# Kernel optimization log

Measured on AMD Instinct MI355X. Metric: run time of the kernel, lower is better.

Reference implementation:

```python
import math
import jax, jax.numpy as jnp
import numpy as np

# hyperparameters (module defaults; w_scale overridden to 1.0)
EMA_SPEED = 0.05
REW_SENS = 1.0
LR = 0.0033
MOMENTUM = 0.4
UNTANH = 0.6
SPEED = 0.5
WIDTH = 0.1
WD = 0.01
LAT_DECAY = 0.01
NOISE_SCALE = 0.8
C_MOMENT = 0.99
W_SCALE = 1.0


def rms_norm(x, axis=-1):
    return x * jax.lax.rsqrt(jnp.mean(x * x, axis=axis, keepdims=True) + 1e-6)


def setup_inputs() -> dict:
    key = jax.random.key(0)
    ks = jax.random.split(key, 16)
    B, N, D = 16, 128, 64
    s = 1.0 / math.sqrt(D)
    return {
        'eye_env': jax.random.normal(ks[0], (B, D), jnp.float32),
        'stomach_env': jax.random.normal(ks[1], (B, D), jnp.float32),
        'state': jax.random.normal(ks[2], (B, N, D), jnp.float32),
        'output': jax.random.normal(ks[3], (B, N, D), jnp.float32),
        'W1': jax.random.normal(ks[4], (B, N, D, D), jnp.float32) * s,
        'W2': jax.random.normal(ks[5], (B, N, D, D), jnp.float32) * s,
        'W3': jax.random.normal(ks[6], (B, N, D, D), jnp.float32) * s,
        'M1': jax.random.normal(ks[7], (B, N, D, D), jnp.float32) * 0.2,
        'M2': jax.random.normal(ks[8], (B, N, D, D), jnp.float32) * 0.2,
        'M3': jax.random.normal(ks[9], (B, N, D, D), jnp.float32) * 0.2,
        'E_baseline': jax.random.uniform(ks[10], (B, N, D), jnp.float32),
        'A': jax.nn.softmax(jax.random.normal(ks[11], (B, N, N), jnp.float32), axis=2),
        'noise_A': jax.random.normal(ks[12], (B, N, N), jnp.float32),
        'noise1_raw': jax.random.normal(ks[13], (B, N, D), jnp.float32),
        'noise2_raw': jax.random.normal(ks[14], (B, N, D), jnp.float32),
        'step_counter': 0,
    }


def reference(eye_env, stomach_env, state, output, W1, W2, W3, M1, M2, M3,
              E_baseline, A, noise_A, noise1_raw, noise2_raw, step_counter):
    B, N, D = state.shape
    sc = jnp.float32(step_counter) + 1.0  # self.step_counter += 1

    # attention routing
    q = jnp.einsum('bnj,bnjk->bnk', state, W3)
    k = jnp.einsum('bnj,bnjk->bnk', state, W2)
    raw_A = jnp.einsum('bnd,bmd->bnm', q, k) / math.sqrt(D) + noise_A * 1e-5
    P_dense = jax.nn.softmax(raw_A, axis=2)
    keep = (P_dense > 1.0 / (N + 1.0)) | (P_dense == jnp.max(P_dense, axis=2, keepdims=True))
    P = jax.nn.softmax(jnp.where(keep, raw_A, -jnp.inf), axis=2)
    A_new = A * C_MOMENT + P * (1.0 - C_MOMENT)
    A_new = A_new.at[:, 0:2, :].set(0.0)

    # message passing + sensory clamp
    target = jnp.einsum('bnm,bmd->bnd', A_new, output)
    target = target.at[:, 0].set(eye_env).at[:, 1].set(stomach_env)

    # prediction
    raw_pred = jnp.einsum('bnj,bnjk->bnk', state, W1)
    raw = raw_pred - jnp.tanh(raw_pred) * UNTANH
    prediction = jnp.tanh(raw) * math.sqrt(2.0 + math.sqrt(2.0))

    err = prediction - target
    E_curr = jax.nn.softmax(err, axis=-1)
    bmask = (E_baseline == 0).astype(jnp.float32)
    Eb = E_baseline * (1.0 - bmask) + E_curr * bmask
    Eb = Eb * (1.0 - EMA_SPEED) + EMA_SPEED * E_curr
    advantage = E_curr - Eb
    R = -rms_norm(advantage[..., None] * REW_SENS)  # (B,N,D,1)
    mask = (Eb > 0).astype(jnp.float32)[..., None]

    # noise injection
    state_mag = jnp.sum(jnp.abs(state), axis=(-2, -1), keepdims=True)
    noise1 = noise1_raw / (1.0 + state_mag)
    noise2 = noise2_raw * jnp.std(err, ddof=1) * NOISE_SCALE
    noisy_state = state + noise1 + noise2

    # Hebbian outer-product gradient, G_NORM=1.0 -> rms-normalized
    lg = -jnp.einsum('bni,bnj->bnij', err, noisy_state)
    lg = rms_norm(lg, axis=(2, 3))

    plasticity = 1.0 - R
    grad1 = plasticity * lg * mask + LAT_DECAY * W3 - WD * W1
    grad2 = plasticity * lg * mask + LAT_DECAY * W1 - WD * W2
    grad3 = plasticity * lg * mask + LAT_DECAY * W2 - WD * W3

    # travelling gaussian column mask
    idx = jnp.arange(D, dtype=jnp.float32).reshape(1, 1, 1, D)
    center = (sc * SPEED) % D
    diff = jnp.abs(idx - center)
    diff = jnp.minimum(diff, D - diff)
    g_mask = jnp.exp(-diff ** 2 / (2.0 * WIDTH ** 2 + 1e-6))

    M1n = M1 * MOMENTUM + (1.0 - MOMENTUM) * (grad1 * g_mask)
    M2n = M2 * MOMENTUM + (1.0 - MOMENTUM) * (grad2 * g_mask)
    M3n = M3 * MOMENTUM + (1.0 - MOMENTUM) * (grad3 * g_mask)
    W1n = rms_norm(W1 + LR * M1n) * W_SCALE
    W2n = rms_norm(W2 + LR * M2n) * W_SCALE
    W3n = rms_norm(W3 + LR * M3n) * W_SCALE

    # new output = prediction, new state = target
    return prediction, target, A_new, W1n, W2n, W3n
```

## Files before the change

kernel.cpp:

```cpp
#include <hip/hip_runtime.h>
#include <hip/hip_bf16.h>

typedef __hip_bfloat16 bf16;
typedef float f32x4 __attribute__((ext_vector_type(4)));

__device__ __forceinline__ float b2f(bf16 x) { return __bfloat162float(x); }

template<bool F32>
__device__ __forceinline__ float ld(const void* p, size_t i) {
  if constexpr (F32) return ((const float*)p)[i];
  else return b2f(((const bf16*)p)[i]);
}

template<bool F32>
__device__ __forceinline__ void ld4(const void* p, size_t i, float v[4]) {
  if constexpr (F32) {
    const float4 a = *(const float4*)((const float*)p + i);
    v[0]=a.x; v[1]=a.y; v[2]=a.z; v[3]=a.w;
  } else {
    union { uint2 u; bf16 h[4]; } t;
    t.u = *(const uint2*)((const bf16*)p + i);
    #pragma unroll
    for (int c = 0; c < 4; ++c) v[c] = b2f(t.h[c]);
  }
}

template<bool F32>
__device__ __forceinline__ void ld8(const void* p, size_t i, float v[8]) {
  if constexpr (F32) {
    const float4 a = *(const float4*)((const float*)p + i);
    const float4 b = *(const float4*)((const float*)p + i + 4);
    v[0]=a.x; v[1]=a.y; v[2]=a.z; v[3]=a.w;
    v[4]=b.x; v[5]=b.y; v[6]=b.z; v[7]=b.w;
  } else {
    union { uint4 u; bf16 h[8]; } t;
    t.u = *(const uint4*)((const bf16*)p + i);
    #pragma unroll
    for (int c = 0; c < 8; ++c) v[c] = b2f(t.h[c]);
  }
}

template<bool F32>
__device__ __forceinline__ void ld8nt(const void* p, size_t i, float v[8]) {
  if constexpr (F32) {
    const f32x4* q = (const f32x4*)((const float*)p + i);
    const f32x4 a = __builtin_nontemporal_load(q);
    const f32x4 b = __builtin_nontemporal_load(q + 1);
    v[0]=a[0]; v[1]=a[1]; v[2]=a[2]; v[3]=a[3];
    v[4]=b[0]; v[5]=b[1]; v[6]=b[2]; v[7]=b[3];
  } else {
    ld8<false>(p, i, v);
  }
}

__device__ __forceinline__ float plast(float Ec, float Ebl) {
  const float Eb0 = (Ebl == 0.f) ? Ec : Ebl;
  const float Eb  = Eb0 * 0.95f + 0.05f * Ec;
  const float adv = Ec - Eb;
  const float R   = -adv * rsqrtf(adv*adv + 1e-6f);
  return (Eb > 0.f) ? (1.f - R) : 0.f;
}


template<bool F32>
__device__ __forceinline__ void k1_wave(
    const void* state, const void* W1, const void* W2, const void* W3,
    float* qw, float* kw, float* mag, float* out_pred, int node, int lane)
{
  const int b = node >> 7;
  const float st = ld<F32>(state, (size_t)node*64 + lane);
  float am = fabsf(st);
  #pragma unroll
  for (int s = 32; s; s >>= 1) am += __shfl_xor(am, s, 64);
  if (lane == 0) atomicAdd(&mag[b], am);

  const int jg = lane >> 4, cq = lane & 15;
  const int c0 = cq * 4;
  const size_t nb = (size_t)node * 4096;
  float aq[4] = {0,0,0,0}, ak[4] = {0,0,0,0}, ap[4] = {0,0,0,0};
  #pragma unroll 4
  for (int jj = 0; jj < 16; ++jj) {
    const int j = jg*16 + jj;
    const float sj = __shfl(st, j, 64);
    const size_t o = nb + (size_t)j*64 + c0;
    float wv[4];
    ld4<F32>(W3, o, wv);
    #pragma unroll
    for (int cc = 0; cc < 4; ++cc) aq[cc] += sj * wv[cc];
    ld4<F32>(W2, o, wv);
    #pragma unroll
    for (int cc = 0; cc < 4; ++cc) ak[cc] += sj * wv[cc];
    ld4<F32>(W1, o, wv);
    #pragma unroll
    for (int cc = 0; cc < 4; ++cc) ap[cc] += sj * wv[cc];
  }
  #pragma unroll
  for (int cc = 0; cc < 4; ++cc) {
    aq[cc] += __shfl_xor(aq[cc], 16, 64); aq[cc] += __shfl_xor(aq[cc], 32, 64);
    ak[cc] += __shfl_xor(ak[cc], 16, 64); ak[cc] += __shfl_xor(ak[cc], 32, 64);
    ap[cc] += __shfl_xor(ap[cc], 16, 64); ap[cc] += __shfl_xor(ap[cc], 32, 64);
  }
  if (jg == 0) {
    *(float4*)(qw + (size_t)node*64 + c0) = make_float4(aq[0], aq[1], aq[2], aq[3]);
  } else if (jg == 1) {
    *(float4*)(kw + (size_t)node*64 + c0) = make_float4(ak[0], ak[1], ak[2], ak[3]);
  } else if (jg == 2) {
    float pr[4];
    #pragma unroll
    for (int cc = 0; cc < 4; ++cc) {
      const float raw = ap[cc] - tanhf(ap[cc]) * 0.6f;
      pr[cc] = tanhf(raw) * 1.8477590650225735f;
    }
    *(float4*)(out_pred + (size_t)node*64 + c0) = make_float4(pr[0], pr[1], pr[2], pr[3]);
  }
}

__global__ __launch_bounds__(256) void k1_qkpred(
    const void* __restrict__ state,
    const void* __restrict__ W1, const void* __restrict__ W2,
    const void* __restrict__ W3,
    float* __restrict__ qw, float* __restrict__ kw,
    float* __restrict__ mag, float* __restrict__ out_pred,
    int* __restrict__ flagws)
{
  const int tid = threadIdx.x;
  const int w = tid >> 6, lane = tid & 63;
  bool huge = false;
  for (int i = lane; i < 1024; i += 64) {
    const float x = b2f(((const bf16*)state)[i]);
    if (!(fabsf(x) < 1e5f)) huge = true;
  }
  const bool f32 = (__ballot(huge) != 0ull);
  if (blockIdx.x == 0 && tid == 0) *flagws = f32 ? 1 : 0;
  const int node = blockIdx.x * 4 + w;
  if (f32) k1_wave<true >(state, W1, W2, W3, qw, kw, mag, out_pred, node, lane);
  else     k1_wave<false>(state, W1, W2, W3, qw, kw, mag, out_pred, node, lane);
}

template<bool F32>
__device__ __forceinline__ void k2_body(
    const float* qw, const float* kw, const float* predw,
    const void* noiseA, const void* Aold, const void* outp,
    const void* eye, const void* stomach, const void* Ebase,
    float* errw, float* plw, float* stats,
    float* out_target, float* out_A,
    float* s_k, float* s_q, float* s_A)
{
  const int bidx = blockIdx.x;
  const int b = bidx >> 4;
  const int n0 = (bidx & 15) * 8;
  const int tid = threadIdx.x;

  {
    const float* kwb = kw + (size_t)b * 8192;
    #pragma unroll
    for (int it = 0; it < 8; ++it) {
      const int idx = it*256 + tid;
      const int m = idx >> 4, dq = idx & 15;
      const float4 v = *(const float4*)(kwb + (size_t)idx * 4);
      float* dst = &s_k[m*65 + dq*4];
      dst[0] = v.x; dst[1] = v.y; dst[2] = v.z; dst[3] = v.w;
    }
    if (tid < 128) {
      const int rr = tid >> 4, dq = tid & 15;
      *(float4*)&s_q[rr*64 + dq*4] =
          *(const float4*)(qw + ((size_t)(b*128 + n0 + rr))*64 + dq*4);
    }
  }
  __syncthreads();

  const int rr = tid >> 5, c = tid & 31;
  const int n = n0 + rr;
  const size_t node = (size_t)b*128 + n;

  float acc[4] = {0.f, 0.f, 0.f, 0.f};
  {
    const float* qrow = s_q + rr*64;
    #pragma unroll 8
    for (int j = 0; j < 64; ++j) {
      const float qv = qrow[j];
      acc[0] += qv * s_k[(c     )*65 + j];
      acc[1] += qv * s_k[(c + 32)*65 + j];
      acc[2] += qv * s_k[(c + 64)*65 + j];
      acc[3] += qv * s_k[(c + 96)*65 + j];
    }
  }
  float raw[4];
  #pragma unroll
  for (int i = 0; i < 4; ++i)
    raw[i] = acc[i]*0.125f + 1e-5f*ld<F32>(noiseA, node*128 + c + 32*i);

  float rmx = fmaxf(fmaxf(raw[0], raw[1]), fmaxf(raw[2], raw[3]));
  #pragma unroll
  for (int s = 16; s >= 1; s >>= 1) rmx = fmaxf(rmx, __shfl_xor(rmx, s, 64));
  float e[4], S = 0.f;
  #pragma unroll
  for (int i = 0; i < 4; ++i) { e[i] = expf(raw[i] - rmx); S += e[i]; }
  #pragma unroll
  for (int s = 16; s >= 1; s >>= 1) S += __shfl_xor(S, s, 64);
  float ek[4], Sk = 0.f;
  #pragma unroll
  for (int i = 0; i < 4; ++i) {
    const float Pd = e[i] / S;
    ek[i] = ((Pd > 0.007751937984496124f) || (raw[i] == rmx)) ? e[i] : 0.f;
    Sk += ek[i];
  }
  #pragma unroll
  for (int s = 16; s >= 1; s >>= 1) Sk += __shfl_xor(Sk, s, 64);
  #pragma unroll
  for (int i = 0; i < 4; ++i) {
    const int m = c + 32*i;
    const float P = ek[i] / Sk;
    const float An = (n < 2) ? 0.f
                   : 0.99f * ld<F32>(Aold, node*128 + m) + 0.01f * P;
    out_A[node*128 + m] = An;
    s_A[rr*128 + m] = An;
  }
  __syncthreads();

  float t0, t1;
  if (n == 0) {
    t0 = ld<F32>(eye, (size_t)b*64 + c);
    t1 = ld<F32>(eye, (size_t)b*64 + c + 32);
  } else if (n == 1) {
    t0 = ld<F32>(stomach, (size_t)b*64 + c);
    t1 = ld<F32>(stomach, (size_t)b*64 + c + 32);
  } else {
    t0 = 0.f; t1 = 0.f;
    const float* arow = s_A + rr*128;
    const size_t ob = (size_t)b * 8192;
    #pragma unroll 4
    for (int m = 0; m < 128; ++m) {
      const float a = arow[m];
      t0 += a * ld<F32>(outp, ob + m*64 + c);
      t1 += a * ld<F32>(outp, ob + m*64 + c + 32);
    }
  }
  out_target[node*64 + c]      = t0;
  out_target[node*64 + c + 32] = t1;
  const float e0 = predw[node*64 + c]      - t0;
  const float e1 = predw[node*64 + c + 32] - t1;
  errw[node*64 + c]      = e0;
  errw[node*64 + c + 32] = e1;

  float mx = fmaxf(e0, e1);
  #pragma unroll
  for (int s = 16; s >= 1; s >>= 1) mx = fmaxf(mx, __shfl_xor(mx, s, 64));
  const float x0 = expf(e0 - mx), x1 = expf(e1 - mx);
  float ss = x0 + x1;
  #pragma unroll
  for (int s = 16; s >= 1; s >>= 1) ss += __shfl_xor(ss, s, 64);
  plw[node*64 + c]      = plast(x0/ss, ld<F32>(Ebase, node*64 + c));
  plw[node*64 + c + 32] = plast(x1/ss, ld<F32>(Ebase, node*64 + c + 32));

  float se = e0 + e1, sq = e0*e0 + e1*e1;
  #pragma unroll
  for (int s = 16; s >= 1; s >>= 1) { se += __shfl_xor(se, s, 64); sq += __shfl_xor(sq, s, 64); }
  if (c == 0) { atomicAdd(&stats[0], se); atomicAdd(&stats[1], sq); }
}

__global__ __launch_bounds__(256) void k2_attn(
    const int* __restrict__ flag,
    const float* __restrict__ qw, const float* __restrict__ kw,
    const float* __restrict__ predw,
    const void* __restrict__ noiseA, const void* __restrict__ Aold,
    const void* __restrict__ outp,
    const void* __restrict__ eye, const void* __restrict__ stomach,
    const void* __restrict__ Ebase,
    float* __restrict__ errw, float* __restrict__ plw,
    float* __restrict__ stats,
    float* __restrict__ out_target, float* __restrict__ out_A)
{
  __shared__ alignas(16) float s_k[128*65];
  __shared__ alignas(16) float s_q[8*64];
  __shared__ alignas(16) float s_A[8*128];
  if (*flag) k2_body<true >(qw,kw,predw,noiseA,Aold,outp,eye,stomach,Ebase,errw,plw,stats,out_target,out_A,s_k,s_q,s_A);
  else       k2_body<false>(qw,kw,predw,noiseA,Aold,outp,eye,stomach,Ebase,errw,plw,stats,out_target,out_A,s_k,s_q,s_A);
}

template<bool F32>
__device__ __forceinline__ void k3_body(
    const float* errw, const float* plw,
    const void* state, const void* n1raw, const void* n2raw,
    const float* mag, const float* stats, const int* stepc,
    const void* W1, const void* W2, const void* W3,
    const void* M1, const void* M2, const void* M3,
    float* oW1, float* oW2, float* oW3)
{
  const int node = blockIdx.x;
  const int b = node >> 7;
  const int tid = threadIdx.x;
  const int lane = tid & 63;
  const int r = tid >> 3;
  const int l8 = tid & 7;

  const size_t sb = (size_t)node*64 + lane;
  const float e_i  = errw[sb];
  const float pl_i = plw[sb];
  const float st_i = ld<F32>(state, sb);
  const float n1_i = ld<F32>(n1raw, sb);
  const float n2_i = ld<F32>(n2raw, sb);
  const float magb = mag[b];
  const float S1 = stats[0], S2 = stats[1];
  const float scv = (float)stepc[0] + 1.f;

  const size_t off = (size_t)node*4096 + (size_t)r*64 + (size_t)l8*8;
  float w1v[8], w2v[8], w3v[8], m1v[8], m2v[8], m3v[8];
  ld8  <F32>(W1, off, w1v); ld8  <F32>(W2, off, w2v); ld8  <F32>(W3, off, w3v);
  ld8nt<F32>(M1, off, m1v); ld8nt<F32>(M2, off, m2v); ld8nt<F32>(M3, off, m3v);

  const float Mn = 131072.f;
  const float var = (S2 - S1*S1/Mn) / (Mn - 1.f);
  const float stdv = sqrtf(fmaxf(var, 0.f));
  const float ns_i = st_i + n1_i / (1.f + magb)
                   + n2_i * stdv * 0.8f;
  float e2 = e_i*e_i, q2 = ns_i*ns_i;
  #pragma unroll
  for (int s = 32; s; s >>= 1) { e2 += __shfl_xor(e2, s, 64); q2 += __shfl_xor(q2, s, 64); }
  const float c_i  = -ns_i * rsqrtf(e2 * q2 * (1.f/4096.f) + 1e-6f);
  const float pe_i = pl_i * e_i;
  const float center = fmodf(scv * 0.5f, 64.f);
  float dff = fabsf((float)lane - center);
  dff = fminf(dff, 64.f - dff);
  const float g_i = expf(-dff*dff * (1.f/0.020001f));

  const float pe = __shfl(pe_i, r, 64);
  float cj[8], gj[8];
  #pragma unroll
  for (int cc = 0; cc < 8; ++cc) {
    const int j = l8*8 + cc;
    cj[cc] = __shfl(c_i, j, 64);
    gj[cc] = __shfl(g_i, j, 64);
  }

  float t1[8], t2[8], t3[8];
  float ss1 = 0.f, ss2 = 0.f, ss3 = 0.f;
  #pragma unroll
  for (int cc = 0; cc < 8; ++cc) {
    const float lgterm = pe * cj[cc];
    const float g = gj[cc];
    const float g1 = lgterm + 0.01f*w3v[cc] - 0.01f*w1v[cc];
    const float g2 = lgterm + 0.01f*w1v[cc] - 0.01f*w2v[cc];
    const float g3 = lgterm + 0.01f*w2v[cc] - 0.01f*w3v[cc];
    const float v1 = w1v[cc] + 0.0033f*(0.4f*m1v[cc] + 0.6f*g1*g);
    const float v2 = w2v[cc] + 0.0033f*(0.4f*m2v[cc] + 0.6f*g2*g);
    const float v3 = w3v[cc] + 0.0033f*(0.4f*m3v[cc] + 0.6f*g3*g);
    t1[cc] = v1; t2[cc] = v2; t3[cc] = v3;
    ss1 += v1*v1; ss2 += v2*v2; ss3 += v3*v3;
  }
  #pragma unroll
  for (int s = 1; s <= 4; s <<= 1) {
    ss1 += __shfl_xor(ss1, s, 64);
    ss2 += __shfl_xor(ss2, s, 64);
    ss3 += __shfl_xor(ss3, s, 64);
  }
  const float r1 = rsqrtf(ss1*(1.f/64.f) + 1e-6f);
  const float r2 = rsqrtf(ss2*(1.f/64.f) + 1e-6f);
  const float r3 = rsqrtf(ss3*(1.f/64.f) + 1e-6f);
  *(float4*)(oW1 + off)     = make_float4(t1[0]*r1, t1[1]*r1, t1[2]*r1, t1[3]*r1);
  *(float4*)(oW1 + off + 4) = make_float4(t1[4]*r1, t1[5]*r1, t1[6]*r1, t1[7]*r1);
  *(float4*)(oW2 + off)     = make_float4(t2[0]*r2, t2[1]*r2, t2[2]*r2, t2[3]*r2);
  *(float4*)(oW2 + off + 4) = make_float4(t2[4]*r2, t2[5]*r2, t2[6]*r2, t2[7]*r2);
  *(float4*)(oW3 + off)     = make_float4(t3[0]*r3, t3[1]*r3, t3[2]*r3, t3[3]*r3);
  *(float4*)(oW3 + off + 4) = make_float4(t3[4]*r3, t3[5]*r3, t3[6]*r3, t3[7]*r3);
}

__global__ __launch_bounds__(512) void k3_update(
    const int* __restrict__ flag,
    const float* __restrict__ errw, const float* __restrict__ plw,
    const void* __restrict__ state, const void* __restrict__ n1raw,
    const void* __restrict__ n2raw,
    const float* __restrict__ mag, const float* __restrict__ stats,
    const int* __restrict__ stepc,
    const void* __restrict__ W1, const void* __restrict__ W2,
    const void* __restrict__ W3,
    const void* __restrict__ M1, const void* __restrict__ M2,
    const void* __restrict__ M3,
    float* __restrict__ oW1, float* __restrict__ oW2, float* __restrict__ oW3)
{
  if (*flag) k3_body<true >(errw,plw,state,n1raw,n2raw,mag,stats,stepc,W1,W2,W3,M1,M2,M3,oW1,oW2,oW3);
  else       k3_body<false>(errw,plw,state,n1raw,n2raw,mag,stats,stepc,W1,W2,W3,M1,M2,M3,oW1,oW2,oW3);
}

extern "C" void kernel_launch(void* const* d_in, const int* in_sizes, int n_in,
                              void* d_out, int out_size, void* d_ws, size_t ws_size,
                              hipStream_t stream) {
  const void* eye     = d_in[0];
  const void* stomach = d_in[1];
  const void* state   = d_in[2];
  const void* outp    = d_in[3];
  const void* W1      = d_in[4];
  const void* W2      = d_in[5];
  const void* W3      = d_in[6];
  const void* M1      = d_in[7];
  const void* M2      = d_in[8];
  const void* M3      = d_in[9];
  const void* Ebase   = d_in[10];
  const void* Aold    = d_in[11];
  const void* noiseA  = d_in[12];
  const void* n1raw   = d_in[13];
  const void* n2raw   = d_in[14];
  const int*  stepc   = (const int*)d_in[15];

  float* ws    = (float*)d_ws;
  float* qw    = ws;
  float* kw    = ws + 131072;
  float* errw  = ws + 262144;
  float* plw   = ws + 393216;
  float* mag   = ws + 524288;
  float* stats = ws + 524304;
  int*   flag  = (int*)(ws + 524306);

  float* out        = (float*)d_out;
  float* out_pred   = out;
  float* out_target = out + 131072;
  float* out_A      = out + 262144;
  float* oW1        = out + 524288;
  float* oW2        = out + 8912896;
  float* oW3        = out + 17301504;

  hipMemsetAsync(mag, 0, 18 * sizeof(float), stream);
  k1_qkpred<<<512, 256, 0, stream>>>(state, W1, W2, W3, qw, kw, mag, out_pred, flag);
  k2_attn<<<256, 256, 0, stream>>>(flag, qw, kw, out_pred, noiseA, Aold, outp,
                                   eye, stomach, Ebase, errw, plw, stats,
                                   out_target, out_A);
  k3_update<<<2048, 512, 0, stream>>>(flag, errw, plw, state, n1raw, n2raw, mag, stats,
                                      stepc, W1, W2, W3, M1, M2, M3, oW1, oW2, oW3);
}
```

Baseline: 358.6 us.

## Split qk/pred projection into one wave per matrix and drop memset

The first kernel now assigns one wave per (node, matrix) pair, launching three times as many blocks. Each lane issues eight vector loads before consuming them, to raise memory-level parallelism on the W reads. The per-batch |state| sum no longer uses atomics: each node writes its own partial, and the attention kernel reduces the partials. The stats accumulators are zeroed inside the first kernel, which removes the separate memset launch. In exchange, every wave reloads and reshuffles state, and more waves are launched.

After: 333.3 us. 1.08x faster.

```diff
diff --git a/kernel.cpp b/kernel.cpp
--- a/kernel.cpp
+++ b/kernel.cpp
@@ -65,53 +65,56 @@
 template<bool F32>
 __device__ __forceinline__ void k1_wave(
     const void* state, const void* W1, const void* W2, const void* W3,
-    float* qw, float* kw, float* mag, float* out_pred, int node, int lane)
-{
-  const int b = node >> 7;
+    float* qw, float* kw, float* magn, float* out_pred,
+    int node, int mat, int lane)
+{
   const float st = ld<F32>(state, (size_t)node*64 + lane);
-  float am = fabsf(st);
-  #pragma unroll
-  for (int s = 32; s; s >>= 1) am += __shfl_xor(am, s, 64);
-  if (lane == 0) atomicAdd(&mag[b], am);
-
   const int jg = lane >> 4, cq = lane & 15;
   const int c0 = cq * 4;
-  const size_t nb = (size_t)node * 4096;
-  float aq[4] = {0,0,0,0}, ak[4] = {0,0,0,0}, ap[4] = {0,0,0,0};
-  #pragma unroll 4
-  for (int jj = 0; jj < 16; ++jj) {
-    const int j = jg*16 + jj;
-    const float sj = __shfl(st, j, 64);
-    const size_t o = nb + (size_t)j*64 + c0;
-    float wv[4];
-    ld4<F32>(W3, o, wv);
-    #pragma unroll
-    for (int cc = 0; cc < 4; ++cc) aq[cc] += sj * wv[cc];
-    ld4<F32>(W2, o, wv);
-    #pragma unroll
-    for (int cc = 0; cc < 4; ++cc) ak[cc] += sj * wv[cc];
-    ld4<F32>(W1, o, wv);
-    #pragma unroll
-    for (int cc = 0; cc < 4; ++cc) ap[cc] += sj * wv[cc];
+  const size_t nb = (size_t)node*4096 + (size_t)jg*1024 + c0;
+  const void* W = (mat == 0) ? W3 : (mat == 1) ? W2 : W1;
+
+  float acc[4] = {0.f, 0.f, 0.f, 0.f};
+  float buf[8][4];
+  #pragma unroll
+  for (int jj = 0; jj < 8; ++jj) ld4<F32>(W, nb + (size_t)jj*64, buf[jj]);
+  #pragma unroll
+  for (int jj = 0; jj < 8; ++jj) {
+    const float sj = __shfl(st, jg*16 + jj, 64);
+    #pragma unroll
+    for (int cc = 0; cc < 4; ++cc) acc[cc] += sj * buf[jj][cc];
+  }
+  #pragma unroll
+  for (int jj = 0; jj < 8; ++jj) ld4<F32>(W, nb + (size_t)(jj + 8)*64, buf[jj]);
+  #pragma unroll
+  for (int jj = 0; jj < 8; ++jj) {
+    const float sj = __shfl(st, jg*16 + 8 + jj, 64);
+    #pragma unroll
+    for (int cc = 0; cc < 4; ++cc) acc[cc] += sj * buf[jj][cc];
   }
   #pragma unroll
   for (int cc = 0; cc < 4; ++cc) {
-    aq[cc] += __shfl_xor(aq[cc], 16, 64); aq[cc] += __shfl_xor(aq[cc], 32, 64);
-    ak[cc] += __shfl_xor(ak[cc], 16, 64); ak[cc] += __shfl_xor(ak[cc], 32, 64);
-    ap[cc] += __shfl_xor(ap[cc], 16, 64); ap[cc] += __shfl_xor(ap[cc], 32, 64);
-  }
-  if (jg == 0) {
-    *(float4*)(qw + (size_t)node*64 + c0) = make_float4(aq[0], aq[1], aq[2], aq[3]);
-  } else if (jg == 1) {
-    *(float4*)(kw + (size_t)node*64 + c0) = make_float4(ak[0], ak[1], ak[2], ak[3]);
-  } else if (jg == 2) {
-    float pr[4];
-    #pragma unroll
-    for (int cc = 0; cc < 4; ++cc) {
-      const float raw = ap[cc] - tanhf(ap[cc]) * 0.6f;
-      pr[cc] = tanhf(raw) * 1.8477590650225735f;
+    acc[cc] += __shfl_xor(acc[cc], 16, 64);
+    acc[cc] += __shfl_xor(acc[cc], 32, 64);
+  }
+
+  if (mat == 2) {
+    float am = fabsf(st);
+    #pragma unroll
+    for (int s = 32; s; s >>= 1) am += __shfl_xor(am, s, 64);
+    if (lane == 0) magn[node] = am;
+    if (jg == 0) {
+      float pr[4];
+      #pragma unroll
+      for (int cc = 0; cc < 4; ++cc) {
+        const float raw = acc[cc] - tanhf(acc[cc]) * 0.6f;
+        pr[cc] = tanhf(raw) * 1.8477590650225735f;
+      }
+      *(float4*)(out_pred + (size_t)node*64 + c0) = make_float4(pr[0], pr[1], pr[2], pr[3]);
     }
-    *(float4*)(out_pred + (size_t)node*64 + c0) = make_float4(pr[0], pr[1], pr[2], pr[3]);
+  } else if (jg == 0) {
+    float* dst = (mat == 0) ? qw : kw;
+    *(float4*)(dst + (size_t)node*64 + c0) = make_float4(acc[0], acc[1], acc[2], acc[3]);
   }
 }
 
@@ -120,8 +123,8 @@
     const void* __restrict__ W1, const void* __restrict__ W2,
     const void* __restrict__ W3,
     float* __restrict__ qw, float* __restrict__ kw,
-    float* __restrict__ mag, float* __restrict__ out_pred,
-    int* __restrict__ flagws)
+    float* __restrict__ magn, float* __restrict__ out_pred,
+    int* __restrict__ flagws, float* __restrict__ stats)
 {
   const int tid = threadIdx.x;
   const int w = tid >> 6, lane = tid & 63;
@@ -131,10 +134,14 @@
     if (!(fabsf(x) < 1e5f)) huge = true;
   }
   const bool f32 = (__ballot(huge) != 0ull);
-  if (blockIdx.x == 0 && tid == 0) *flagws = f32 ? 1 : 0;
-  const int node = blockIdx.x * 4 + w;
-  if (f32) k1_wave<true >(state, W1, W2, W3, qw, kw, mag, out_pred, node, lane);
-  else     k1_wave<false>(state, W1, W2, W3, qw, kw, mag, out_pred, node, lane);
+  if (blockIdx.x == 0 && tid == 0) {
+    *flagws = f32 ? 1 : 0;
+    stats[0] = 0.f; stats[1] = 0.f;
+  }
+  const int wid = blockIdx.x * 4 + w;
+  const int node = wid & 2047, mat = wid >> 11;
+  if (f32) k1_wave<true >(state, W1, W2, W3, qw, kw, magn, out_pred, node, mat, lane);
+  else     k1_wave<false>(state, W1, W2, W3, qw, kw, magn, out_pred, node, mat, lane);
 }
 
 template<bool F32>
@@ -142,6 +149,7 @@
     const float* qw, const float* kw, const float* predw,
     const void* noiseA, const void* Aold, const void* outp,
     const void* eye, const void* stomach, const void* Ebase,
+    const float* magn, float* mag,
     float* errw, float* plw, float* stats,
     float* out_target, float* out_A,
     float* s_k, float* s_q, float* s_A)
@@ -150,6 +158,13 @@
   const int b = bidx >> 4;
   const int n0 = (bidx & 15) * 8;
   const int tid = threadIdx.x;
+
+  if (n0 == 0 && tid < 64) {
+    float v = magn[b*128 + tid] + magn[b*128 + 64 + tid];
+    #pragma unroll
+    for (int s = 32; s; s >>= 1) v += __shfl_xor(v, s, 64);
+    if (tid == 0) mag[b] = v;
+  }
 
   {
     const float* kwb = kw + (size_t)b * 8192;
@@ -267,6 +282,7 @@
     const void* __restrict__ outp,
     const void* __restrict__ eye, const void* __restrict__ stomach,
     const void* __restrict__ Ebase,
+    const float* __restrict__ magn, float* __restrict__ mag,
     float* __restrict__ errw, float* __restrict__ plw,
     float* __restrict__ stats,
     float* __restrict__ out_target, float* __restrict__ out_A)
@@ -274,8 +290,8 @@
   __shared__ alignas(16) float s_k[128*65];
   __shared__ alignas(16) float s_q[8*64];
   __shared__ alignas(16) float s_A[8*128];
-  if (*flag) k2_body<true >(qw,kw,predw,noiseA,Aold,outp,eye,stomach,Ebase,errw,plw,stats,out_target,out_A,s_k,s_q,s_A);
-  else       k2_body<false>(qw,kw,predw,noiseA,Aold,outp,eye,stomach,Ebase,errw,plw,stats,out_target,out_A,s_k,s_q,s_A);
+  if (*flag) k2_body<true >(qw,kw,predw,noiseA,Aold,outp,eye,stomach,Ebase,magn,mag,errw,plw,stats,out_target,out_A,s_k,s_q,s_A);
+  else       k2_body<false>(qw,kw,predw,noiseA,Aold,outp,eye,stomach,Ebase,magn,mag,errw,plw,stats,out_target,out_A,s_k,s_q,s_A);
 }
 
 template<bool F32>
@@ -407,9 +423,10 @@
   float* kw    = ws + 131072;
   float* errw  = ws + 262144;
   float* plw   = ws + 393216;
-  float* mag   = ws + 524288;
-  float* stats = ws + 524304;
-  int*   flag  = (int*)(ws + 524306);
+  float* magn  = ws + 524288;
+  float* mag   = ws + 526336;
+  float* stats = ws + 526352;
+  int*   flag  = (int*)(ws + 526354);
 
   float* out        = (float*)d_out;
   float* out_pred   = out;
@@ -419,10 +436,10 @@
   float* oW2        = out + 8912896;
   float* oW3        = out + 17301504;
 
-  hipMemsetAsync(mag, 0, 18 * sizeof(float), stream);
-  k1_qkpred<<<512, 256, 0, stream>>>(state, W1, W2, W3, qw, kw, mag, out_pred, flag);
+  k1_qkpred<<<1536, 256, 0, stream>>>(state, W1, W2, W3, qw, kw, magn, out_pred,
+                                      flag, stats);
   k2_attn<<<256, 256, 0, stream>>>(flag, qw, kw, out_pred, noiseA, Aold, outp,
-                                   eye, stomach, Ebase, errw, plw, stats,
+                                   eye, stomach, Ebase, magn, mag, errw, plw, stats,
                                    out_target, out_A);
   k3_update<<<2048, 512, 0, stream>>>(flag, errw, plw, state, n1raw, n2raw, mag, stats,
                                       stepc, W1, W2, W3, M1, M2, M3, oW1, oW2, oW3);
```
